# Optimization experiments

Hardware: AMD Instinct MI355X
Metric: run time of the kernel (lower is better)

## Reference

```python
import jax, jax.numpy as jnp
import numpy as np

HEADS = 8
DEPTH = 4
DIM = 128
FF_DIM = 4 * DIM
EPS = 1e-5


def _layer_norm(x, g, b):
    m = jnp.mean(x, axis=-1, keepdims=True)
    v = jnp.mean(jnp.square(x - m), axis=-1, keepdims=True)
    return (x - m) * jax.lax.rsqrt(v + EPS) * g + b


def _linear_attn(x, Wq, Wk, Wv, Wo, bo):
    # lucidrains linear-attention-transformer global (non-causal) linear attention
    b, n, d = x.shape
    dh = d // HEADS
    q = (x @ Wq).reshape(b, n, HEADS, dh).transpose(0, 2, 1, 3)  # bhnd
    k = (x @ Wk).reshape(b, n, HEADS, dh).transpose(0, 2, 1, 3)
    v = (x @ Wv).reshape(b, n, HEADS, dh).transpose(0, 2, 1, 3)
    q = jax.nn.softmax(q, axis=-1) * (dh ** -0.5)  # softmax over feature dim
    k = jax.nn.softmax(k, axis=2)                  # softmax over sequence dim
    ctx = jnp.einsum('bhnd,bhne->bhde', k, v)      # [b,h,dh,dh]
    o = jnp.einsum('bhnd,bhde->bhne', q, ctx)
    o = o.transpose(0, 2, 1, 3).reshape(b, n, d)
    return o @ Wo + bo


def _ff(x, W1, b1, W2, b2):
    return jax.nn.gelu(x @ W1 + b1) @ W2 + b2


def _stack(x, p):
    Wq, Wk, Wv, Wo, bo, g1, be1, g2, be2, W1, bf1, W2, bf2 = p
    for i in range(DEPTH):  # fixed small depth, structurally distinct params
        x = x + _linear_attn(_layer_norm(x, g1[i], be1[i]), Wq[i], Wk[i], Wv[i], Wo[i], bo[i])
        x = x + _ff(_layer_norm(x, g2[i], be2[i]), W1[i], bf1[i], W2[i], bf2[i])
    return x


def _make_stack_params(key):
    ks = jax.random.split(key, 6)
    w = lambda k, s: jax.random.normal(k, s, jnp.float32) * 0.02
    return dict(
        Wq=w(ks[0], (DEPTH, DIM, DIM)), Wk=w(ks[1], (DEPTH, DIM, DIM)),
        Wv=w(ks[2], (DEPTH, DIM, DIM)), Wo=w(ks[3], (DEPTH, DIM, DIM)),
        bo=jnp.zeros((DEPTH, DIM), jnp.float32),
        g1=jnp.ones((DEPTH, DIM), jnp.float32), be1=jnp.zeros((DEPTH, DIM), jnp.float32),
        g2=jnp.ones((DEPTH, DIM), jnp.float32), be2=jnp.zeros((DEPTH, DIM), jnp.float32),
        W1=w(ks[4], (DEPTH, DIM, FF_DIM)), bf1=jnp.zeros((DEPTH, FF_DIM), jnp.float32),
        W2=w(ks[5], (DEPTH, FF_DIM, DIM)), bf2=jnp.zeros((DEPTH, DIM), jnp.float32),
    )


def setup_inputs() -> dict:
    key = jax.random.key(0)
    kx, kc, kt = jax.random.split(key, 3)
    x = jax.random.normal(kx, (64, DIM, 62, 64), jnp.float32)  # [B, emb, num_chan, num_patch]
    pc = {k + '_c': v for k, v in _make_stack_params(kc).items()}
    pt = {k + '_t': v for k, v in _make_stack_params(kt).items()}
    return {'x': x, **pc, **pt}


def reference(x,
              Wq_c, Wk_c, Wv_c, Wo_c, bo_c, g1_c, be1_c, g2_c, be2_c, W1_c, bf1_c, W2_c, bf2_c,
              Wq_t, Wk_t, Wv_t, Wo_t, bo_t, g1_t, be1_t, g2_t, be2_t, W1_t, bf1_t, W2_t, bf2_t):
    b, e, c, p = x.shape
    h = jnp.transpose(x, (0, 3, 2, 1)).reshape(b * p, c, e)  # [B*P, C, E] channel attention
    h = _stack(h, (Wq_c, Wk_c, Wv_c, Wo_c, bo_c, g1_c, be1_c, g2_c, be2_c, W1_c, bf1_c, W2_c, bf2_c)).mean(1)
    h = h.reshape(b, p, e)                                   # [B, P, E] temporal attention
    h = _stack(h, (Wq_t, Wk_t, Wv_t, Wo_t, bo_t, g1_t, be1_t, g2_t, be2_t, W1_t, bf1_t, W2_t, bf2_t)).mean(1)
    return h
```

## Files before the change

### kernel.cpp

```cpp
#include <hip/hip_runtime.h>
#include <stdint.h>

typedef unsigned short u16;
typedef unsigned int   u32;
typedef __attribute__((ext_vector_type(8))) short short8;
typedef __attribute__((ext_vector_type(4))) float f32x4;

#define HEADS  8
#define DH     16
#define DIM    128
#define FFD    512
#define NDEPTH 4
#define NEPS   1e-5f
#define NT     256
#define NTP    256
#define LDA    136

#define U_N     23040
#define BK_OFF  2048
#define KT_OFF  2048
#define VT_OFF  10240
#define BK2_OFF 14336

__device__ __forceinline__ float bf2f(u16 u) { return __uint_as_float(((u32)u) << 16); }
__device__ __forceinline__ u16 f2bf(float f) {
    u32 u = __float_as_uint(f);
    u32 r = (u + 0x7FFFu + ((u >> 16) & 1u)) >> 16;
    return (u16)r;
}

template <typename T> struct VT;
template <> struct VT<u16> {
    static __device__ __forceinline__ float ld(const u16* p) { return bf2f(*p); }
    static __device__ __forceinline__ void st(u16* p, float v) { *p = f2bf(v); }
};
template <> struct VT<float> {
    static __device__ __forceinline__ float ld(const float* p) { return *p; }
    static __device__ __forceinline__ void st(float* p, float v) { *p = v; }
};

struct SPv { const void* q[13]; };
struct WTs { const u16 *q, *k, *v, *o, *w1, *w2; };

template <typename T> struct SP {
    const T *bo, *g1, *be1, *g2, *be2, *bf1, *bf2;
    __device__ __forceinline__ SP(const SPv& s) {
        bo = (const T*)s.q[4];  g1 = (const T*)s.q[5];  be1 = (const T*)s.q[6];
        g2 = (const T*)s.q[7];  be2 = (const T*)s.q[8]; bf1 = (const T*)s.q[10];
        bf2 = (const T*)s.q[12];
    }
};

__device__ __forceinline__ void zero_acc(f32x4 acc[4][2]) {
    #pragma unroll
    for (int i = 0; i < 4; ++i)
        #pragma unroll
        for (int j = 0; j < 2; ++j) {
            acc[i][j].x = 0.f; acc[i][j].y = 0.f; acc[i][j].z = 0.f; acc[i][j].w = 0.f;
        }
}

__device__ __forceinline__ void gemm_lds(const u16* Ab, const u16* WT, int Ks,
                                         int nc0, int lane, f32x4 acc[4][2]) {
    const int n = lane & 15, quad = lane >> 4;
    #pragma unroll
    for (int ks = 0; ks < 4; ++ks) {
        short8 b0 = *(const short8*)(WT + (size_t)(nc0 + n) * Ks + ks * 32 + quad * 8);
        short8 b1 = *(const short8*)(WT + (size_t)(nc0 + 16 + n) * Ks + ks * 32 + quad * 8);
        #pragma unroll
        for (int mt = 0; mt < 4; ++mt) {
            short8 a = *(const short8*)(Ab + (mt * 16 + n) * LDA + ks * 32 + quad * 8);
            acc[mt][0] = __builtin_amdgcn_mfma_f32_16x16x32_bf16(a, b0, acc[mt][0], 0, 0, 0);
            acc[mt][1] = __builtin_amdgcn_mfma_f32_16x16x32_bf16(a, b1, acc[mt][1], 0, 0, 0);
        }
    }
}

__device__ __forceinline__ void store_bf16_tile(u16* dst, const f32x4 acc[4][2],
                                                int nc0, int lane) {
    const int c = lane & 15, quad = lane >> 4;
    #pragma unroll
    for (int mt = 0; mt < 4; ++mt)
        #pragma unroll
        for (int nt = 0; nt < 2; ++nt) {
            const float* a = (const float*)&acc[mt][nt];
            #pragma unroll
            for (int r = 0; r < 4; ++r)
                dst[(mt * 16 + quad * 4 + r) * LDA + nc0 + nt * 16 + c] = f2bf(a[r]);
        }
}

template <int MV, typename T>
__device__ __forceinline__ void ln_frag(const f32x4 (&h)[4][2], u16* yb, float* red,
                                        const T* g, const T* be,
                                        int lane, int quad, int nc0, int wn) {
    const int cid = lane & 15;
    const int col0 = nc0 + cid, col1 = col0 + 16;
    #pragma unroll
    for (int mt = 0; mt < 4; ++mt) {
        float s1[4], s2[4];
        #pragma unroll
        for (int r = 0; r < 4; ++r) {
            float a = h[mt][0][r], b = h[mt][1][r];
            s1[r] = a + b;
            s2[r] = fmaf(a, a, b * b);
        }
        #pragma unroll
        for (int m = 1; m <= 8; m <<= 1)
            #pragma unroll
            for (int r = 0; r < 4; ++r) {
                s1[r] += __shfl_xor(s1[r], m, 64);
                s2[r] += __shfl_xor(s2[r], m, 64);
            }
        if (cid == 0) {
            #pragma unroll
            for (int r = 0; r < 4; ++r) {
                const int row = mt * 16 + quad * 4 + r;
                red[row * 8 + wn]     = s1[r];
                red[row * 8 + 4 + wn] = s2[r];
            }
        }
    }
    __syncthreads();
    const float gl0 = VT<T>::ld(g + col0), gl1 = VT<T>::ld(g + col1);
    const float bl0 = VT<T>::ld(be + col0), bl1 = VT<T>::ld(be + col1);
    #pragma unroll
    for (int mt = 0; mt < 4; ++mt)
        #pragma unroll
        for (int r = 0; r < 4; ++r) {
            const int row = mt * 16 + quad * 4 + r;
            float4 p1 = *(const float4*)&red[row * 8];
            float4 p2 = *(const float4*)&red[row * 8 + 4];
            float t1 = (p1.x + p1.y) + (p1.z + p1.w);
            float t2 = (p2.x + p2.y) + (p2.z + p2.w);
            float mean = t1 * (1.0f / 128.0f);
            float var  = fmaxf(t2 * (1.0f / 128.0f) - mean * mean, 0.0f);
            float rstd = rsqrtf(var + NEPS);
            const bool valid = row < MV;
            float o0 = valid ? fmaf((h[mt][0][r] - mean) * rstd, gl0, bl0) : 0.0f;
            float o1 = valid ? fmaf((h[mt][1][r] - mean) * rstd, gl1, bl1) : 0.0f;
            yb[row * LDA + col0] = f2bf(o0);
            yb[row * LDA + col1] = f2bf(o1);
        }
    __syncthreads();
}

template <int MV>
__device__ __forceinline__ void ksoftmax_reg(f32x4 (&acc)[4][2], int lane) {
    const int quad = lane >> 4;
    #pragma unroll
    for (int nt = 0; nt < 2; ++nt) {
        float mx = -1e30f;
        #pragma unroll
        for (int mt = 0; mt < 4; ++mt)
            #pragma unroll
            for (int r = 0; r < 4; ++r) {
                const int lrow = mt * 16 + quad * 4 + r;
                mx = fmaxf(mx, (lrow < MV) ? acc[mt][nt][r] : -1e30f);
            }
        mx = fmaxf(mx, __shfl_xor(mx, 16, 64));
        mx = fmaxf(mx, __shfl_xor(mx, 32, 64));
        float s = 0.0f;
        #pragma unroll
        for (int mt = 0; mt < 4; ++mt)
            #pragma unroll
            for (int r = 0; r < 4; ++r) {
                const int lrow = mt * 16 + quad * 4 + r;
                float e = (lrow < MV) ? __expf(acc[mt][nt][r] - mx) : 0.0f;
                acc[mt][nt][r] = e;
                s += e;
            }
        s += __shfl_xor(s, 16, 64);
        s += __shfl_xor(s, 32, 64);
        const float inv = __builtin_amdgcn_rcpf(s);
        #pragma unroll
        for (int mt = 0; mt < 4; ++mt)
            #pragma unroll
            for (int r = 0; r < 4; ++r)
                acc[mt][nt][r] *= inv;
    }
}

__device__ __forceinline__ void qsoftmax_scale(f32x4 (&acc)[4][2], int lane) {
    (void)lane;
    #pragma unroll
    for (int mt = 0; mt < 4; ++mt)
        #pragma unroll
        for (int nt = 0; nt < 2; ++nt)
            #pragma unroll
            for (int r = 0; r < 4; ++r) {
                float e = __expf(acc[mt][nt][r]);
                float s = e;
                s += __shfl_xor(s, 1, 64);
                s += __shfl_xor(s, 2, 64);
                s += __shfl_xor(s, 4, 64);
                s += __shfl_xor(s, 8, 64);
                acc[mt][nt][r] = e * (0.25f * __builtin_amdgcn_rcpf(s));
            }
}

__device__ __forceinline__ int swzk(int row, int n) {
    return ((row << 7) | (n << 1)) ^ ((row & 7) << 4);
}
__device__ __forceinline__ int swzb(int row, int n) {
    return ((row << 6) | (n << 1)) ^ ((row & 3) << 4);
}

template <int C>
__device__ __forceinline__ void store_kT_chunk(const f32x4 (&a)[4][2], u16* Th,
                                               int lane, int nc0) {
    const int cid = lane & 15, quad = lane >> 4;
    #pragma unroll
    for (int m = 0; m < 2; ++m)
        #pragma unroll
        for (int nt = 0; nt < 2; ++nt) {
            const int row = nc0 + nt * 16 + cid;
            #pragma unroll
            for (int rr = 0; rr < 2; ++rr) {
                const int n = C * 32 + m * 16 + quad * 4 + rr * 2;
                u32 w = (u32)f2bf(a[C * 2 + m][nt][rr * 2]) |
                        ((u32)f2bf(a[C * 2 + m][nt][rr * 2 + 1]) << 16);
                *(u32*)((char*)Th + swzk(row, n)) = w;
            }
        }
}

template <int C>
__device__ __forceinline__ void store_vT_chunk(const f32x4 (&a)[4][2], u16* Th,
                                               int lane, int nc0) {
    const int cid = lane & 15, quad = lane >> 4;
    #pragma unroll
    for (int m = 0; m < 2; ++m)
        #pragma unroll
        for (int nt = 0; nt < 2; ++nt) {
            const int row = nc0 + nt * 16 + cid;
            #pragma unroll
            for (int rr = 0; rr < 2; ++rr) {
                const int n = m * 16 + quad * 4 + rr * 2;
                u32 w = (u32)f2bf(a[C * 2 + m][nt][rr * 2]) |
                        ((u32)f2bf(a[C * 2 + m][nt][rr * 2 + 1]) << 16);
                *(u32*)((char*)Th + swzb(row, n)) = w;
            }
        }
}

template <int C>
__device__ __forceinline__ void ctx_chunk(const u16* kTs, const u16* vTs,
                                          f32x4 (&ctxacc)[2], int lane, int wn) {
    const int cid = lane & 15, quad = lane >> 4;
    #pragma unroll
    for (int h01 = 0; h01 < 2; ++h01) {
        const int row = (wn * 2 + h01) * 16 + cid;
        short8 a = *(const short8*)((const char*)vTs + swzb(row, quad * 8));
        short8 b = *(const short8*)((const char*)kTs + swzk(row, C * 32 + quad * 8));
        ctxacc[h01] = __builtin_amdgcn_mfma_f32_16x16x32_bf16(a, b, ctxacc[h01], 0, 0, 0);
    }
}

__device__ __forceinline__ void o_mfma(u16* qb, const u16* ctxs, int wn, int lane) {
    const int cid = lane & 15, quad = lane >> 4;
    f32x4 z; z.x = 0.f; z.y = 0.f; z.z = 0.f; z.w = 0.f;
    #pragma unroll
    for (int h01 = 0; h01 < 2; ++h01) {
        const int hd = wn * 2 + h01;
        short8 b = {0, 0, 0, 0, 0, 0, 0, 0};
        if (quad < 2)
            b = *(const short8*)(ctxs + hd * 256 + cid * 16 + quad * 8);
        #pragma unroll
        for (int mt = 0; mt < 4; ++mt) {
            short8 a = *(const short8*)(qb + (mt * 16 + cid) * LDA + hd * DH + (quad & 1) * 8);
            f32x4 o = __builtin_amdgcn_mfma_f32_16x16x32_bf16(a, b, z, 0, 0, 0);
            #pragma unroll
            for (int r = 0; r < 4; ++r)
                qb[(mt * 16 + quad * 4 + r) * LDA + hd * DH + cid] = f2bf(o[r]);
        }
    }
}

__device__ __forceinline__ float gelu_f(float v) {
    float u = 0.7978845608028654f * fmaf(0.044715f * v, v * v, v);
    u = fminf(fmaxf(u, -20.0f), 20.0f);
    float e  = __expf(2.0f * u);
    float th = 1.0f - 2.0f * __builtin_amdgcn_rcpf(e + 1.0f);
    return 0.5f * v * (1.0f + th);
}

template <typename T>
__device__ __forceinline__ void gelu_store(const f32x4 (&acc)[4][2], u16* dst,
                                           const T* bf1, int col0, int col1,
                                           int quad) {
    const float b10 = VT<T>::ld(bf1 + col0);
    const float b11 = VT<T>::ld(bf1 + col1);
    #pragma unroll
    for (int mt = 0; mt < 4; ++mt)
        #pragma unroll
        for (int r = 0; r < 4; ++r) {
            const int row = mt * 16 + quad * 4 + r;
            dst[row * LDA + col0] = f2bf(gelu_f(acc[mt][0][r] + b10));
            dst[row * LDA + col1] = f2bf(gelu_f(acc[mt][1][r] + b11));
        }
}

template <int MV, typename T>
__device__ __forceinline__ void run_stack(f32x4 (&h)[4][2], u16* yb, u16* U16,
                                          const WTs& wt, const SP<T>& p) {
    const int tid = threadIdx.x;
    const int lane = tid & 63, wn = tid >> 6;
    const int quad = lane >> 4, cid = lane & 15;
    const int nc0 = wn * 32;
    const int col0 = nc0 + cid, col1 = col0 + 16;
    float* red  = (float*)U16;
    u16*   bKa  = U16 + BK_OFF;
    u16*   bKb  = U16 + BK2_OFF;
    u16*   kTs  = U16 + KT_OFF;
    u16*   vTs  = U16 + VT_OFF;
    u16*   ctxs = U16;

    for (int L = 0; L < NDEPTH; ++L) {
        const u16* WqT = wt.q + L * 16384;
        const u16* WkT = wt.k + L * 16384;
        const u16* WvT = wt.v + L * 16384;
        const u16* WoT = wt.o + L * 16384;
        const u16* W1T = wt.w1 + L * 65536;
        const u16* W2T = wt.w2 + L * 65536;

        ln_frag<MV, T>(h, yb, red, p.g1 + L * DIM, p.be1 + L * DIM, lane, quad, nc0, wn);

        f32x4 acc[4][2];
        zero_acc(acc);
        gemm_lds(yb, WkT, DIM, nc0, lane, acc);
        ksoftmax_reg<MV>(acc, lane);
        store_kT_chunk<0>(acc, kTs, lane, nc0);
        store_kT_chunk<1>(acc, kTs, lane, nc0);
        zero_acc(acc);
        gemm_lds(yb, WvT, DIM, nc0, lane, acc);
        f32x4 ctxacc[2];
        #pragma unroll
        for (int i = 0; i < 2; ++i) {
            ctxacc[i].x = 0.f; ctxacc[i].y = 0.f; ctxacc[i].z = 0.f; ctxacc[i].w = 0.f;
        }
        store_vT_chunk<0>(acc, vTs, lane, nc0);
        ctx_chunk<0>(kTs, vTs, ctxacc, lane, wn);
        store_vT_chunk<1>(acc, vTs, lane, nc0);
        ctx_chunk<1>(kTs, vTs, ctxacc, lane, wn);
        #pragma unroll
        for (int h01 = 0; h01 < 2; ++h01)
            #pragma unroll
            for (int r = 0; r < 4; ++r)
                ctxs[(wn * 2 + h01) * 256 + (quad * 4 + r) * 16 + cid] = f2bf(ctxacc[h01][r]);

        zero_acc(acc);
        gemm_lds(yb, WqT, DIM, nc0, lane, acc);
        qsoftmax_scale(acc, lane);
        __syncthreads();
        store_bf16_tile(bKa, acc, nc0, lane);
        o_mfma(bKa, ctxs, wn, lane);
        __syncthreads();

        gemm_lds(bKa, WoT, DIM, nc0, lane, h);
        {
            const float b0 = VT<T>::ld(p.bo + L * DIM + col0);
            const float b1 = VT<T>::ld(p.bo + L * DIM + col1);
            #pragma unroll
            for (int mt = 0; mt < 4; ++mt)
                #pragma unroll
                for (int r = 0; r < 4; ++r) { h[mt][0][r] += b0; h[mt][1][r] += b1; }
        }

        ln_frag<MV, T>(h, yb, red, p.g2 + L * DIM, p.be2 + L * DIM, lane, quad, nc0, wn);

        zero_acc(acc);
        gemm_lds(yb, W1T, DIM, nc0, lane, acc);
        gelu_store(acc, bKa, p.bf1 + L * FFD, col0, col1, quad);
        __syncthreads();
        #pragma unroll
        for (int cc = 0; cc < 4; ++cc) {
            u16* cur = (cc & 1) ? bKb : bKa;
            u16* nxt = (cc & 1) ? bKa : bKb;
            if (cc < 3) {
                zero_acc(acc);
                gemm_lds(yb, W1T + (cc + 1) * 128 * DIM, DIM, nc0, lane, acc);
            }
            gemm_lds(cur, W2T + cc * 128, FFD, nc0, lane, h);
            if (cc < 3) {
                gelu_store(acc, nxt, p.bf1 + L * FFD + (cc + 1) * 128, col0, col1, quad);
                __syncthreads();
            }
        }
        {
            const float b0 = VT<T>::ld(p.bf2 + L * DIM + col0);
            const float b1 = VT<T>::ld(p.bf2 + L * DIM + col1);
            #pragma unroll
            for (int mt = 0; mt < 4; ++mt)
                #pragma unroll
                for (int r = 0; r < 4; ++r) { h[mt][0][r] += b0; h[mt][1][r] += b1; }
        }
    }
}

__device__ __forceinline__ bool is_bf16_g(const void* g1) {
    return *reinterpret_cast<const u32*>(g1) == 0x3F803F80u;
}

template <typename T>
__device__ __forceinline__ void channel_body(const T* x, const float* xT, int xmode,
                                             const SPv& pv, const WTs& wt,
                                             float* pooled, u16* yb, u16* U16) {
    SP<T> p(pv);
    const int tid = threadIdx.x;
    const int lane = tid & 63, wn = tid >> 6;
    const int quad = lane >> 4, cid = lane & 15;
    const int nc0 = wn * 32;
    const int col0 = nc0 + cid, col1 = col0 + 16;
    const int seq = blockIdx.x;

    f32x4 h[4][2];
    if (xmode) {
        const float* xrow = xT + (size_t)seq * 62 * DIM;
        #pragma unroll
        for (int mt = 0; mt < 4; ++mt)
            #pragma unroll
            for (int r = 0; r < 4; ++r) {
                const int row = mt * 16 + quad * 4 + r;
                h[mt][0][r] = (row < 62) ? xrow[row * DIM + col0] : 0.0f;
                h[mt][1][r] = (row < 62) ? xrow[row * DIM + col1] : 0.0f;
            }
    } else {
        const int b = seq >> 6, pp = seq & 63;
        #pragma unroll
        for (int mt = 0; mt < 4; ++mt)
            #pragma unroll
            for (int r = 0; r < 4; ++r) {
                const int row = mt * 16 + quad * 4 + r;
                h[mt][0][r] = (row < 62)
                    ? VT<T>::ld(x + (((size_t)b * DIM + col0) * 62 + row) * 64 + pp) : 0.0f;
                h[mt][1][r] = (row < 62)
                    ? VT<T>::ld(x + (((size_t)b * DIM + col1) * 62 + row) * 64 + pp) : 0.0f;
            }
    }

    run_stack<62, T>(h, yb, U16, wt, p);

    float s0 = 0.0f, s1 = 0.0f;
    #pragma unroll
    for (int mt = 0; mt < 4; ++mt)
        #pragma unroll
        for (int r = 0; r < 4; ++r) {
            const int row = mt * 16 + quad * 4 + r;
            if (row < 62) { s0 += h[mt][0][r]; s1 += h[mt][1][r]; }
        }
    s0 += __shfl_xor(s0, 16, 64); s0 += __shfl_xor(s0, 32, 64);
    s1 += __shfl_xor(s1, 16, 64); s1 += __shfl_xor(s1, 32, 64);
    if (quad == 0) {
        pooled[(size_t)seq * DIM + col0] = s0 * (1.0f / 62.0f);
        pooled[(size_t)seq * DIM + col1] = s1 * (1.0f / 62.0f);
    }
}

template <typename T>
__device__ __forceinline__ void temporal_body(const float* pooled, const SPv& pv,
                                              const WTs& wt, T* out, u16* yb, u16* U16) {
    SP<T> p(pv);
    const int tid = threadIdx.x;
    const int lane = tid & 63, wn = tid >> 6;
    const int quad = lane >> 4, cid = lane & 15;
    const int nc0 = wn * 32;
    const int col0 = nc0 + cid, col1 = col0 + 16;
    const int seq = blockIdx.x;

    f32x4 h[4][2];
    #pragma unroll
    for (int mt = 0; mt < 4; ++mt)
        #pragma unroll
        for (int r = 0; r < 4; ++r) {
            const int row = mt * 16 + quad * 4 + r;
            h[mt][0][r] = pooled[((size_t)seq * 64 + row) * DIM + col0];
            h[mt][1][r] = pooled[((size_t)seq * 64 + row) * DIM + col1];
        }

    run_stack<64, T>(h, yb, U16, wt, p);

    float s0 = 0.0f, s1 = 0.0f;
    #pragma unroll
    for (int mt = 0; mt < 4; ++mt)
        #pragma unroll
        for (int r = 0; r < 4; ++r) { s0 += h[mt][0][r]; s1 += h[mt][1][r]; }
    s0 += __shfl_xor(s0, 16, 64); s0 += __shfl_xor(s0, 32, 64);
    s1 += __shfl_xor(s1, 16, 64); s1 += __shfl_xor(s1, 32, 64);
    if (quad == 0) {
        VT<T>::st(out + (size_t)seq * DIM + col0, s0 * (1.0f / 64.0f));
        VT<T>::st(out + (size_t)seq * DIM + col1, s1 * (1.0f / 64.0f));
    }
}

__global__ __launch_bounds__(NT, 2) void k_channel(const void* xv, const float* xT,
                                                   int xmode, SPv pv, WTs wt,
                                                   float* __restrict__ pooled) {
    __shared__ __attribute__((aligned(16))) u16 yb[64 * LDA];
    __shared__ __attribute__((aligned(16))) u16 Ubuf[U_N];

    if (is_bf16_g(pv.q[5]))
        channel_body<u16>((const u16*)xv, xT, xmode, pv, wt, pooled, yb, Ubuf);
    else
        channel_body<float>((const float*)xv, xT, xmode, pv, wt, pooled, yb, Ubuf);
}

__global__ __launch_bounds__(NT, 2) void k_temporal(const float* __restrict__ pooled,
                                                    SPv pv, WTs wt, void* outv) {
    __shared__ __attribute__((aligned(16))) u16 yb[64 * LDA];
    __shared__ __attribute__((aligned(16))) u16 Ubuf[U_N];

    if (is_bf16_g(pv.q[5]))
        temporal_body<u16>(pooled, pv, wt, (u16*)outv, yb, Ubuf);
    else
        temporal_body<float>(pooled, pv, wt, (float*)outv, yb, Ubuf);
}

template <typename T>
__device__ __forceinline__ void prepx_body(const T* x, float* xT, float* t) {
    const int tid = threadIdx.x;
    const int b = blockIdx.x >> 3, cg = blockIdx.x & 7;
    const int c1 = (cg == 7) ? 62 : (cg * 8 + 8);
    for (int c = cg * 8; c < c1; ++c) {
        #pragma unroll 4
        for (int rep = 0; rep < 32; ++rep) {
            const int idx = rep * NTP + tid;
            const int e = idx >> 6, pp = idx & 63;
            t[pp * 132 + e] = VT<T>::ld(x + (((size_t)b * DIM + e) * 62 + c) * 64 + pp);
        }
        __syncthreads();
        #pragma unroll 4
        for (int rep = 0; rep < 32; ++rep) {
            const int idx = rep * NTP + tid;
            const int pp = idx >> 7, e = idx & 127;
            xT[((size_t)(b * 64 + pp) * 62 + c) * DIM + e] = t[pp * 132 + e];
        }
        __syncthreads();
    }
}

__global__ __launch_bounds__(NTP) void k_prepx(const void* xv, const void* g1, float* xT) {
    __shared__ float t[64 * 132];
    if (is_bf16_g(g1)) prepx_body<u16>((const u16*)xv, xT, t);
    else               prepx_body<float>((const float*)xv, xT, t);
}

struct TD { const void* src; u16* dst; int K; int N; int nelem; };
struct TDs { TD a[12]; const void* g1; };

__global__ __launch_bounds__(NTP) void k_prep(TDs t) {
    const bool bf = (*(const u32*)t.g1 == 0x3F803F80u);
    int idx = blockIdx.x * NTP + threadIdx.x;
    #pragma unroll 1
    for (int i = 0; i < 12; ++i) {
        if (idx < t.a[i].nelem) {
            const int K = t.a[i].K, N = t.a[i].N;
            const int l = idx / (K * N);
            const int r = idx - l * K * N;
            const int n = r / K;
            const int k = r - n * K;
            const size_t si = ((size_t)l * K + k) * N + n;
            float v = bf ? bf2f(((const u16*)t.a[i].src)[si])
                         : ((const float*)t.a[i].src)[si];
            t.a[i].dst[idx] = f2bf(v);
            return;
        }
        idx -= t.a[i].nelem;
    }
}

extern "C" void kernel_launch(void* const* d_in, const int* in_sizes, int n_in,
                              void* d_out, int out_size, void* d_ws, size_t ws_size,
                              hipStream_t stream) {
    (void)in_sizes; (void)n_in; (void)out_size;
    SPv pc, pt;
    for (int i = 0; i < 13; ++i) pc.q[i] = d_in[1 + i];
    for (int i = 0; i < 13; ++i) pt.q[i] = d_in[14 + i];

    float* pooled = (float*)d_ws;
    u16*   wtb    = (u16*)((char*)d_ws + (size_t)4096 * 128 * 4);
    const size_t XT_OFF = 8u << 20;
    float* xT     = (float*)((char*)d_ws + XT_OFF);
    const size_t xt_need = XT_OFF + (size_t)4096 * 62 * DIM * 4;
    const int xmode = (ws_size >= xt_need) ? 1 : 0;

    const int SQ = 4 * DIM * DIM;
    const int SF = 4 * DIM * FFD;
    const int STK = 4 * SQ + 2 * SF;

    WTs wc { wtb, wtb + SQ, wtb + 2 * SQ, wtb + 3 * SQ, wtb + 4 * SQ, wtb + 4 * SQ + SF };
    u16* wtb2 = wtb + STK;
    WTs wt2 { wtb2, wtb2 + SQ, wtb2 + 2 * SQ, wtb2 + 3 * SQ, wtb2 + 4 * SQ, wtb2 + 4 * SQ + SF };

    TDs td;
    td.a[0]  = { d_in[1],  (u16*)wc.q,  DIM, DIM, SQ };
    td.a[1]  = { d_in[2],  (u16*)wc.k,  DIM, DIM, SQ };
    td.a[2]  = { d_in[3],  (u16*)wc.v,  DIM, DIM, SQ };
    td.a[3]  = { d_in[4],  (u16*)wc.o,  DIM, DIM, SQ };
    td.a[4]  = { d_in[10], (u16*)wc.w1, DIM, FFD, SF };
    td.a[5]  = { d_in[12], (u16*)wc.w2, FFD, DIM, SF };
    td.a[6]  = { d_in[14], (u16*)wt2.q,  DIM, DIM, SQ };
    td.a[7]  = { d_in[15], (u16*)wt2.k,  DIM, DIM, SQ };
    td.a[8]  = { d_in[16], (u16*)wt2.v,  DIM, DIM, SQ };
    td.a[9]  = { d_in[17], (u16*)wt2.o,  DIM, DIM, SQ };
    td.a[10] = { d_in[23], (u16*)wt2.w1, DIM, FFD, SF };
    td.a[11] = { d_in[25], (u16*)wt2.w2, FFD, DIM, SF };
    td.g1 = d_in[6];

    const int total = 2 * STK;
    k_prep<<<dim3((total + NTP - 1) / NTP), dim3(NTP), 0, stream>>>(td);
    if (xmode)
        k_prepx<<<dim3(64 * 8), dim3(NTP), 0, stream>>>(d_in[0], d_in[6], xT);

    k_channel<<<dim3(4096), dim3(NT), 0, stream>>>(d_in[0], xT, xmode, pc, wc, pooled);
    k_temporal<<<dim3(64),  dim3(NT), 0, stream>>>(pooled, pt, wt2, d_out);
}
```

Before: 1.718 ms.

## Fuse K/V projections, defer key-softmax normalization, simplify GELU and reorder LDS buffers

Computes the K and V projections in one pass that shares the A-fragment loads. The key softmax no longer subtracts a max or normalizes per element; the reciprocal sum is applied to the context matrix instead. The Q projection is moved earlier and one __syncthreads is dropped by relocating the bKa buffer so it no longer overlaps kT. GELU's tanh form is rewritten as v*sigmoid(2u) without clamping. These changes raise register pressure from holding two accumulator sets, and dropping the max subtraction risks exp overflow on large logits.

```diff
diff --git a/kernel.cpp b/kernel.cpp
--- a/kernel.cpp
+++ b/kernel.cpp
@@ -17,10 +17,10 @@
 #define LDA    136
 
 #define U_N     23040
-#define BK_OFF  2048
 #define KT_OFF  2048
 #define VT_OFF  10240
-#define BK2_OFF 14336
+#define BK_OFF  14336
+#define BK2_OFF 2048
 
 __device__ __forceinline__ float bf2f(u16 u) { return __uint_as_float(((u32)u) << 16); }
 __device__ __forceinline__ u16 f2bf(float f) {
@@ -72,6 +72,29 @@
             short8 a = *(const short8*)(Ab + (mt * 16 + n) * LDA + ks * 32 + quad * 8);
             acc[mt][0] = __builtin_amdgcn_mfma_f32_16x16x32_bf16(a, b0, acc[mt][0], 0, 0, 0);
             acc[mt][1] = __builtin_amdgcn_mfma_f32_16x16x32_bf16(a, b1, acc[mt][1], 0, 0, 0);
+        }
+    }
+}
+
+__device__ __forceinline__ void gemm2_lds(const u16* Ab, const u16* Wk, const u16* Wv,
+                                          int nc0, int lane,
+                                          f32x4 aK[4][2], f32x4 aV[4][2]) {
+    const int n = lane & 15, quad = lane >> 4;
+    #pragma unroll
+    for (int ks = 0; ks < 4; ++ks) {
+        const size_t o0 = (size_t)(nc0 + n) * DIM + ks * 32 + quad * 8;
+        const size_t o1 = (size_t)(nc0 + 16 + n) * DIM + ks * 32 + quad * 8;
+        short8 bk0 = *(const short8*)(Wk + o0);
+        short8 bk1 = *(const short8*)(Wk + o1);
+        short8 bv0 = *(const short8*)(Wv + o0);
+        short8 bv1 = *(const short8*)(Wv + o1);
+        #pragma unroll
+        for (int mt = 0; mt < 4; ++mt) {
+            short8 a = *(const short8*)(Ab + (mt * 16 + n) * LDA + ks * 32 + quad * 8);
+            aK[mt][0] = __builtin_amdgcn_mfma_f32_16x16x32_bf16(a, bk0, aK[mt][0], 0, 0, 0);
+            aK[mt][1] = __builtin_amdgcn_mfma_f32_16x16x32_bf16(a, bk1, aK[mt][1], 0, 0, 0);
+            aV[mt][0] = __builtin_amdgcn_mfma_f32_16x16x32_bf16(a, bv0, aV[mt][0], 0, 0, 0);
+            aV[mt][1] = __builtin_amdgcn_mfma_f32_16x16x32_bf16(a, bv1, aV[mt][1], 0, 0, 0);
         }
     }
 }
@@ -146,38 +169,23 @@
 }
 
 template <int MV>
-__device__ __forceinline__ void ksoftmax_reg(f32x4 (&acc)[4][2], int lane) {
+__device__ __forceinline__ void ksoftmax_exp(f32x4 (&acc)[4][2], float (&inv)[2], int lane) {
     const int quad = lane >> 4;
     #pragma unroll
     for (int nt = 0; nt < 2; ++nt) {
-        float mx = -1e30f;
+        float s = 0.0f;
         #pragma unroll
         for (int mt = 0; mt < 4; ++mt)
             #pragma unroll
             for (int r = 0; r < 4; ++r) {
                 const int lrow = mt * 16 + quad * 4 + r;
-                mx = fmaxf(mx, (lrow < MV) ? acc[mt][nt][r] : -1e30f);
-            }
-        mx = fmaxf(mx, __shfl_xor(mx, 16, 64));
-        mx = fmaxf(mx, __shfl_xor(mx, 32, 64));
-        float s = 0.0f;
-        #pragma unroll
-        for (int mt = 0; mt < 4; ++mt)
-            #pragma unroll
-            for (int r = 0; r < 4; ++r) {
-                const int lrow = mt * 16 + quad * 4 + r;
-                float e = (lrow < MV) ? __expf(acc[mt][nt][r] - mx) : 0.0f;
+                float e = (lrow < MV) ? __expf(acc[mt][nt][r]) : 0.0f;
                 acc[mt][nt][r] = e;
                 s += e;
             }
         s += __shfl_xor(s, 16, 64);
         s += __shfl_xor(s, 32, 64);
-        const float inv = __builtin_amdgcn_rcpf(s);
-        #pragma unroll
-        for (int mt = 0; mt < 4; ++mt)
-            #pragma unroll
-            for (int r = 0; r < 4; ++r)
-                acc[mt][nt][r] *= inv;
+        inv[nt] = __builtin_amdgcn_rcpf(s);
     }
 }
 
@@ -279,10 +287,8 @@
 
 __device__ __forceinline__ float gelu_f(float v) {
     float u = 0.7978845608028654f * fmaf(0.044715f * v, v * v, v);
-    u = fminf(fmaxf(u, -20.0f), 20.0f);
-    float e  = __expf(2.0f * u);
-    float th = 1.0f - 2.0f * __builtin_amdgcn_rcpf(e + 1.0f);
-    return 0.5f * v * (1.0f + th);
+    float e = __expf(-2.0f * u);
+    return v * __builtin_amdgcn_rcpf(1.0f + e);
 }
 
 template <typename T>
@@ -310,11 +316,11 @@
     const int nc0 = wn * 32;
     const int col0 = nc0 + cid, col1 = col0 + 16;
     float* red  = (float*)U16;
+    u16*   ctxs = U16;
+    u16*   kTs  = U16 + KT_OFF;
+    u16*   vTs  = U16 + VT_OFF;
     u16*   bKa  = U16 + BK_OFF;
     u16*   bKb  = U16 + BK2_OFF;
-    u16*   kTs  = U16 + KT_OFF;
-    u16*   vTs  = U16 + VT_OFF;
-    u16*   ctxs = U16;
 
     for (int L = 0; L < NDEPTH; ++L) {
         const u16* WqT = wt.q + L * 16384;
@@ -326,34 +332,35 @@
 
         ln_frag<MV, T>(h, yb, red, p.g1 + L * DIM, p.be1 + L * DIM, lane, quad, nc0, wn);
 
-        f32x4 acc[4][2];
-        zero_acc(acc);
-        gemm_lds(yb, WkT, DIM, nc0, lane, acc);
-        ksoftmax_reg<MV>(acc, lane);
-        store_kT_chunk<0>(acc, kTs, lane, nc0);
-        store_kT_chunk<1>(acc, kTs, lane, nc0);
-        zero_acc(acc);
-        gemm_lds(yb, WvT, DIM, nc0, lane, acc);
+        f32x4 aK[4][2], aV[4][2];
+        zero_acc(aK);
+        zero_acc(aV);
+        gemm2_lds(yb, WkT, WvT, nc0, lane, aK, aV);
+        float inv[2];
+        ksoftmax_exp<MV>(aK, inv, lane);
+        store_kT_chunk<0>(aK, kTs, lane, nc0);
+        store_kT_chunk<1>(aK, kTs, lane, nc0);
+        f32x4 aQ[4][2];
+        zero_acc(aQ);
+        gemm_lds(yb, WqT, DIM, nc0, lane, aQ);
         f32x4 ctxacc[2];
         #pragma unroll
         for (int i = 0; i < 2; ++i) {
             ctxacc[i].x = 0.f; ctxacc[i].y = 0.f; ctxacc[i].z = 0.f; ctxacc[i].w = 0.f;
         }
-        store_vT_chunk<0>(acc, vTs, lane, nc0);
+        store_vT_chunk<0>(aV, vTs, lane, nc0);
         ctx_chunk<0>(kTs, vTs, ctxacc, lane, wn);
-        store_vT_chunk<1>(acc, vTs, lane, nc0);
+        store_vT_chunk<1>(aV, vTs, lane, nc0);
         ctx_chunk<1>(kTs, vTs, ctxacc, lane, wn);
         #pragma unroll
         for (int h01 = 0; h01 < 2; ++h01)
             #pragma unroll
             for (int r = 0; r < 4; ++r)
-                ctxs[(wn * 2 + h01) * 256 + (quad * 4 + r) * 16 + cid] = f2bf(ctxacc[h01][r]);
-
-        zero_acc(acc);
-        gemm_lds(yb, WqT, DIM, nc0, lane, acc);
-        qsoftmax_scale(acc, lane);
-        __syncthreads();
-        store_bf16_tile(bKa, acc, nc0, lane);
+                ctxs[(wn * 2 + h01) * 256 + (quad * 4 + r) * 16 + cid] =
+                    f2bf(ctxacc[h01][r] * inv[h01]);
+
+        qsoftmax_scale(aQ, lane);
+        store_bf16_tile(bKa, aQ, nc0, lane);
         o_mfma(bKa, ctxs, wn, lane);
         __syncthreads();
 
@@ -369,6 +376,7 @@
 
         ln_frag<MV, T>(h, yb, red, p.g2 + L * DIM, p.be2 + L * DIM, lane, quad, nc0, wn);
 
+        f32x4 acc[4][2];
         zero_acc(acc);
         gemm_lds(yb, W1T, DIM, nc0, lane, acc);
         gelu_store(acc, bKa, p.bf1 + L * FFD, col0, col1, quad);
```

Result: slower. 2.059 ms (+19.8%).

## Defer key-softmax normalization into ctx, simplify GELU, drop a barrier

Applied to the files above, without the earlier changes.

The key softmax no longer subtracts a running max or rescales every element. It keeps only the exp and the per-column reciprocal sum, and applies that reciprocal when the small per-head context matrix is written to LDS. GELU's tanh form becomes the equivalent sigmoid form x*sigmoid(2u), with no clamp. The bK buffer offsets are swapped so the Q tile no longer overlaps the context or kT region, which lets one __syncthreads before storing Q be removed. The risks are overflow from the unstabilised exp on large key logits, and a new buffer-aliasing hazard if the swapped region is still in use elsewhere.

```diff
diff --git a/kernel.cpp b/kernel.cpp
--- a/kernel.cpp
+++ b/kernel.cpp
@@ -17,10 +17,10 @@
 #define LDA    136
 
 #define U_N     23040
-#define BK_OFF  2048
 #define KT_OFF  2048
 #define VT_OFF  10240
-#define BK2_OFF 14336
+#define BK_OFF  14336
+#define BK2_OFF 2048
 
 __device__ __forceinline__ float bf2f(u16 u) { return __uint_as_float(((u32)u) << 16); }
 __device__ __forceinline__ u16 f2bf(float f) {
@@ -146,38 +146,23 @@
 }
 
 template <int MV>
-__device__ __forceinline__ void ksoftmax_reg(f32x4 (&acc)[4][2], int lane) {
+__device__ __forceinline__ void ksoftmax_exp(f32x4 (&acc)[4][2], float (&inv)[2], int lane) {
     const int quad = lane >> 4;
     #pragma unroll
     for (int nt = 0; nt < 2; ++nt) {
-        float mx = -1e30f;
+        float s = 0.0f;
         #pragma unroll
         for (int mt = 0; mt < 4; ++mt)
             #pragma unroll
             for (int r = 0; r < 4; ++r) {
                 const int lrow = mt * 16 + quad * 4 + r;
-                mx = fmaxf(mx, (lrow < MV) ? acc[mt][nt][r] : -1e30f);
-            }
-        mx = fmaxf(mx, __shfl_xor(mx, 16, 64));
-        mx = fmaxf(mx, __shfl_xor(mx, 32, 64));
-        float s = 0.0f;
-        #pragma unroll
-        for (int mt = 0; mt < 4; ++mt)
-            #pragma unroll
-            for (int r = 0; r < 4; ++r) {
-                const int lrow = mt * 16 + quad * 4 + r;
-                float e = (lrow < MV) ? __expf(acc[mt][nt][r] - mx) : 0.0f;
+                float e = (lrow < MV) ? __expf(acc[mt][nt][r]) : 0.0f;
                 acc[mt][nt][r] = e;
                 s += e;
             }
         s += __shfl_xor(s, 16, 64);
         s += __shfl_xor(s, 32, 64);
-        const float inv = __builtin_amdgcn_rcpf(s);
-        #pragma unroll
-        for (int mt = 0; mt < 4; ++mt)
-            #pragma unroll
-            for (int r = 0; r < 4; ++r)
-                acc[mt][nt][r] *= inv;
+        inv[nt] = __builtin_amdgcn_rcpf(s);
     }
 }
 
@@ -279,10 +264,8 @@
 
 __device__ __forceinline__ float gelu_f(float v) {
     float u = 0.7978845608028654f * fmaf(0.044715f * v, v * v, v);
-    u = fminf(fmaxf(u, -20.0f), 20.0f);
-    float e  = __expf(2.0f * u);
-    float th = 1.0f - 2.0f * __builtin_amdgcn_rcpf(e + 1.0f);
-    return 0.5f * v * (1.0f + th);
+    float e = __expf(-2.0f * u);
+    return v * __builtin_amdgcn_rcpf(1.0f + e);
 }
 
 template <typename T>
@@ -310,11 +293,11 @@
     const int nc0 = wn * 32;
     const int col0 = nc0 + cid, col1 = col0 + 16;
     float* red  = (float*)U16;
+    u16*   ctxs = U16;
+    u16*   kTs  = U16 + KT_OFF;
+    u16*   vTs  = U16 + VT_OFF;
     u16*   bKa  = U16 + BK_OFF;
     u16*   bKb  = U16 + BK2_OFF;
-    u16*   kTs  = U16 + KT_OFF;
-    u16*   vTs  = U16 + VT_OFF;
-    u16*   ctxs = U16;
 
     for (int L = 0; L < NDEPTH; ++L) {
         const u16* WqT = wt.q + L * 16384;
@@ -329,7 +312,8 @@
         f32x4 acc[4][2];
         zero_acc(acc);
         gemm_lds(yb, WkT, DIM, nc0, lane, acc);
-        ksoftmax_reg<MV>(acc, lane);
+        float inv[2];
+        ksoftmax_exp<MV>(acc, inv, lane);
         store_kT_chunk<0>(acc, kTs, lane, nc0);
         store_kT_chunk<1>(acc, kTs, lane, nc0);
         zero_acc(acc);
@@ -347,12 +331,12 @@
         for (int h01 = 0; h01 < 2; ++h01)
             #pragma unroll
             for (int r = 0; r < 4; ++r)
-                ctxs[(wn * 2 + h01) * 256 + (quad * 4 + r) * 16 + cid] = f2bf(ctxacc[h01][r]);
+                ctxs[(wn * 2 + h01) * 256 + (quad * 4 + r) * 16 + cid] =
+                    f2bf(ctxacc[h01][r] * inv[h01]);
 
         zero_acc(acc);
         gemm_lds(yb, WqT, DIM, nc0, lane, acc);
         qsoftmax_scale(acc, lane);
-        __syncthreads();
         store_bf16_tile(bKa, acc, nc0, lane);
         o_mfma(bKa, ctxs, wn, lane);
         __syncthreads();
```

Measured after the change: 1.685 ms. About the same (-2.0%).
